# Kernel optimization log

Measured on AMD Instinct MI355X. Metric: run time of the kernel, lower is better.

The kernel has to match this reference:

```python
import jax, jax.numpy as jnp
import numpy as np

N = 100000
E = 1250000
D = 64
EPS = 1e-12


def lgconv(x, edge_index):
    # PyG LGConv: symmetric gcn_norm WITHOUT self-loops, scatter-add to target.
    src, dst = edge_index[0], edge_index[1]
    n = x.shape[0]
    deg = jax.ops.segment_sum(jnp.ones((edge_index.shape[1],), x.dtype), dst, num_segments=n)
    dinv = jnp.where(deg > 0, jax.lax.rsqrt(jnp.maximum(deg, 1.0)) * (deg > 0), 0.0)
    dinv = jnp.where(deg > 0, deg ** -0.5, 0.0)
    norm = dinv[src] * dinv[dst]                      # [E]
    msgs = norm[:, None] * x[src]                     # [E, D]
    return jax.ops.segment_sum(msgs, dst, num_segments=n)


def l2_normalize(x):
    # torch F.normalize(dim=1): x / max(||x||_2, eps)
    nrm = jnp.sqrt(jnp.sum(x * x, axis=1, keepdims=True))
    return x / jnp.maximum(nrm, EPS)


def setup_inputs() -> dict:
    key = jax.random.key(0)
    ks = jax.random.split(key, 8)
    return {
        "init_feat": jax.random.normal(ks[0], (N, D), jnp.float32),
        "W1": jax.random.normal(ks[1], (3 * D, 128), jnp.float32) * (1.0 / np.sqrt(3 * D)),
        "b1": jnp.zeros((128,), jnp.float32),
        "W2": jax.random.normal(ks[2], (128, 3), jnp.float32) * (1.0 / np.sqrt(128)),
        "b2": jnp.zeros((3,), jnp.float32),
        "edge_index_title": jax.random.randint(ks[3], (2, E), 0, N, jnp.int32),
        "edge_index_year": jax.random.randint(ks[4], (2, E), 0, N, jnp.int32),
        "edge_index_cat": jax.random.randint(ks[5], (2, E), 0, N, jnp.int32),
    }


def reference(init_feat, W1, b1, W2, b2, edge_index_title, edge_index_year, edge_index_cat):
    x_title = init_feat
    for _ in range(2):
        x_title = lgconv(x_title, edge_index_title)
    x_title = l2_normalize(x_title)

    x_year = lgconv(init_feat, edge_index_year)
    x_year = l2_normalize(x_year)

    x_cat = init_feat
    for _ in range(3):
        x_cat = lgconv(x_cat, edge_index_cat)
    x_cat = l2_normalize(x_cat)

    x_all = jnp.concatenate([x_title, x_year, x_cat], axis=1)  # [N, 3D]
    h = jax.nn.relu(x_all @ W1 + b1)
    att = jax.nn.softmax(h @ W2 + b2, axis=1)                  # [N, 3]
    out = att[:, 0:1] * x_title + att[:, 1:2] * x_year + att[:, 2:3] * x_cat
    return out
```

## Files before the change

### kernel.cpp

```cpp
#include <hip/hip_runtime.h>


constexpr int NN = 100000;
constexpr int NE = 1250000;
constexpr int BROWS = 128;
constexpr int NB = (NN + BROWS - 1) / BROWS;
constexpr int CHUNK = 8192;
constexpr int NCHUNK = (NE + CHUNK - 1) / CHUNK;

typedef short bf16x8 __attribute__((ext_vector_type(8)));
typedef short bf16x4 __attribute__((ext_vector_type(4)));
typedef float f32x4 __attribute__((ext_vector_type(4)));

__device__ inline short f2bf(float f) {
    unsigned u = __builtin_bit_cast(unsigned, f);
    u += 0x7FFFu + ((u >> 16) & 1u);
    return (short)(u >> 16);
}

__global__ __launch_bounds__(256) void k_bhist(const int* __restrict__ e0, const int* __restrict__ e1,
                                               const int* __restrict__ e2, int* __restrict__ btot) {
    __shared__ int hist[NB];
    const int tid = threadIdx.x;
    const int set = blockIdx.x / NCHUNK;
    const int chunk = blockIdx.x % NCHUNK;
    const int* ei = (set == 0) ? e0 : (set == 1) ? e1 : e2;
    const int ebase = chunk * CHUNK;
    for (int b = tid; b < NB; b += 256) hist[b] = 0;
    __syncthreads();
    #pragma unroll
    for (int j = 0; j < CHUNK / 256; ++j) {
        int e = ebase + tid + j * 256;
        if (e < NE) atomicAdd(&hist[ei[NE + e] >> 7], 1);
    }
    __syncthreads();
    for (int b = tid; b < NB; b += 256) {
        int h = hist[b];
        if (h > 0) atomicAdd(&btot[set * NB + b], h);
    }
}

__global__ __launch_bounds__(256) void k_bscan2(const int* __restrict__ btot,
                                                int* __restrict__ bstart, int* __restrict__ gcur) {
    const int tid = threadIdx.x;
    if (tid >= 64) return;
    for (int s = 0; s < 3; ++s) {
        int run = 0;
        for (int base = 0; base < NB; base += 64) {
            int idx = base + tid;
            int v = (idx < NB) ? btot[s * NB + idx] : 0;
            int incl = v;
            #pragma unroll
            for (int off = 1; off < 64; off <<= 1) {
                int u = __shfl_up(incl, off);
                if (tid >= off) incl += u;
            }
            if (idx < NB) {
                int st = run + incl - v;
                bstart[s * NB + idx] = st;
                gcur[s * NB + idx] = st;
            }
            run += __shfl(incl, 63);
        }
    }
}

__global__ __launch_bounds__(256) void k_bscat(const int* __restrict__ e0, const int* __restrict__ e1,
                                               const int* __restrict__ e2,
                                               int* __restrict__ gcur, int* __restrict__ gpacked) {
    __shared__ int lpack[CHUNK];
    __shared__ unsigned short lbkt[CHUNK];
    __shared__ int hist[NB];
    __shared__ int lbase[NB];
    __shared__ int lcur[NB];
    const int tid = threadIdx.x;
    const int set = blockIdx.x / NCHUNK;
    const int chunk = blockIdx.x % NCHUNK;
    const int* ei = (set == 0) ? e0 : (set == 1) ? e1 : e2;
    const int ebase = chunk * CHUNK;

    for (int b = tid; b < NB; b += 256) { hist[b] = 0; lcur[b] = 0; }
    __syncthreads();

    #pragma unroll
    for (int j = 0; j < CHUNK / 256; ++j) {
        int k = tid + j * 256;
        int e = ebase + k;
        if (e < NE) {
            int s = ei[e];
            int d = ei[NE + e];
            int b = d >> 7;
            lpack[k] = ((d & 127) << 17) | s;
            lbkt[k] = (unsigned short)b;
            atomicAdd(&hist[b], 1);
        } else {
            lbkt[k] = 0xFFFFu;
        }
    }
    __syncthreads();
    for (int b = tid; b < NB; b += 256) {
        int h = hist[b];
        if (h > 0) lbase[b] = atomicAdd(&gcur[set * NB + b], h);
    }
    __syncthreads();
    int* gp = gpacked + (size_t)set * NE;
    #pragma unroll
    for (int j = 0; j < CHUNK / 256; ++j) {
        int k = tid + j * 256;
        unsigned short b = lbkt[k];
        if (b != 0xFFFFu) {
            int pos = lbase[b] + atomicAdd(&lcur[b], 1);
            gp[pos] = lpack[k];
        }
    }
}

__global__ __launch_bounds__(256) void k_bfin(const int* __restrict__ gpacked,
                                              const int* __restrict__ bstart,
                                              const int* __restrict__ gcur,
                                              int* __restrict__ cnt, float* __restrict__ dinv,
                                              int* __restrict__ rowstart, int* __restrict__ csr) {
    __shared__ int hist[BROWS];
    __shared__ int rst[BROWS];
    __shared__ int lcur[BROWS];
    const int tid = threadIdx.x;
    const int set = blockIdx.x / NB, b = blockIdx.x % NB;
    if (tid < BROWS) { hist[tid] = 0; lcur[tid] = 0; }
    __syncthreads();

    const int base = bstart[set * NB + b];
    const int n = gcur[set * NB + b] - base;
    const int* gp = gpacked + (size_t)set * NE + base;

    for (int k = tid; k < n; k += 256) atomicAdd(&hist[(gp[k] >> 17) & 127], 1);
    __syncthreads();

    if (tid < 64) {
        int v0 = hist[tid], v1 = hist[64 + tid];
        int i0 = v0;
        #pragma unroll
        for (int off = 1; off < 64; off <<= 1) {
            int u = __shfl_up(i0, off);
            if (tid >= off) i0 += u;
        }
        int t0 = __shfl(i0, 63);
        int i1 = v1;
        #pragma unroll
        for (int off = 1; off < 64; off <<= 1) {
            int u = __shfl_up(i1, off);
            if (tid >= off) i1 += u;
        }
        rst[tid] = base + i0 - v0;
        rst[64 + tid] = base + t0 + i1 - v1;
    }
    __syncthreads();

    if (tid < BROWS) {
        int node = b * BROWS + tid;
        if (node < NN) {
            int c = hist[tid];
            cnt[set * NN + node] = c;
            dinv[set * NN + node] = (c > 0) ? (1.0f / sqrtf((float)c)) : 0.0f;
            rowstart[set * NN + node] = rst[tid];
        }
    }

    int* cs = csr + (size_t)set * NE;
    for (int k = tid; k < n; k += 256) {
        int p = gp[k];
        int d = (p >> 17) & 127;
        int pos = rst[d] + atomicAdd(&lcur[d], 1);
        cs[pos] = p & 0x1FFFF;
    }
}

__global__ __launch_bounds__(256) void k_prep(const float* __restrict__ W1, short* __restrict__ W1t) {
    int idx = blockIdx.x * 256 + threadIdx.x;
    if (idx < 128 * 192) {
        int n = idx & 127, k = idx >> 7;
        W1t[n * 192 + k] = f2bf(W1[k * 128 + n]);
    }
}

template<bool PRE, bool SQOUT>
__global__ __launch_bounds__(256) void k_gather(const float* __restrict__ x, float* __restrict__ y,
                                                const int* __restrict__ csr, const int* __restrict__ rowstart,
                                                const int* __restrict__ cnt, const float* __restrict__ dinv) {
    const int node = blockIdx.x * 4 + (threadIdx.x >> 6);
    const int lane = threadIdx.x & 63;
    const int sub = lane >> 4;
    const int fq = lane & 15;
    const int n = cnt[node];
    float a0 = 0.f, a1 = 0.f, a2 = 0.f, a3 = 0.f;
    if (n > 0) {
        const int* lst = csr + rowstart[node];
        for (int i = sub; i < n; i += 16) {
            const int j1 = i + 4, j2 = i + 8, j3 = i + 12;
            const int s0 = lst[i];
            const int s1 = lst[j1 < n ? j1 : n - 1];
            const int s2 = lst[j2 < n ? j2 : n - 1];
            const int s3 = lst[j3 < n ? j3 : n - 1];
            float w0, w1, w2, w3;
            if (PRE) {
                w0 = 1.f;
                w1 = (j1 < n) ? 1.f : 0.f;
                w2 = (j2 < n) ? 1.f : 0.f;
                w3 = (j3 < n) ? 1.f : 0.f;
            } else {
                w0 = dinv[s0];
                w1 = (j1 < n) ? dinv[s1] : 0.f;
                w2 = (j2 < n) ? dinv[s2] : 0.f;
                w3 = (j3 < n) ? dinv[s3] : 0.f;
            }
            const float4 v0 = *(const float4*)(x + (size_t)s0 * 64 + fq * 4);
            const float4 v1 = *(const float4*)(x + (size_t)s1 * 64 + fq * 4);
            const float4 v2 = *(const float4*)(x + (size_t)s2 * 64 + fq * 4);
            const float4 v3 = *(const float4*)(x + (size_t)s3 * 64 + fq * 4);
            a0 = fmaf(w0, v0.x, a0); a1 = fmaf(w0, v0.y, a1);
            a2 = fmaf(w0, v0.z, a2); a3 = fmaf(w0, v0.w, a3);
            a0 = fmaf(w1, v1.x, a0); a1 = fmaf(w1, v1.y, a1);
            a2 = fmaf(w1, v1.z, a2); a3 = fmaf(w1, v1.w, a3);
            a0 = fmaf(w2, v2.x, a0); a1 = fmaf(w2, v2.y, a1);
            a2 = fmaf(w2, v2.z, a2); a3 = fmaf(w2, v2.w, a3);
            a0 = fmaf(w3, v3.x, a0); a1 = fmaf(w3, v3.y, a1);
            a2 = fmaf(w3, v3.z, a2); a3 = fmaf(w3, v3.w, a3);
        }
    }
    a0 += __shfl_xor(a0, 16); a1 += __shfl_xor(a1, 16);
    a2 += __shfl_xor(a2, 16); a3 += __shfl_xor(a3, 16);
    a0 += __shfl_xor(a0, 32); a1 += __shfl_xor(a1, 32);
    a2 += __shfl_xor(a2, 32); a3 += __shfl_xor(a3, 32);
    if (sub == 0) {
        float dn = dinv[node];
        float sc = SQOUT ? dn * dn : dn;
        *(float4*)(y + (size_t)node * 64 + fq * 4) =
            make_float4(sc * a0, sc * a1, sc * a2, sc * a3);
    }
}

constexpr int XROW = 200;

__global__ __launch_bounds__(256) void k_final(const float* __restrict__ xt, const float* __restrict__ xy,
                                               const float* __restrict__ xc, const short* __restrict__ W1t,
                                               const float* __restrict__ b1, const float* __restrict__ W2,
                                               const float* __restrict__ b2, float* __restrict__ out) {
    __shared__ alignas(16) short Xn[64 * XROW];
    __shared__ float rnorm[3 * 64];
    __shared__ float attw[64][4];
    const int tid = threadIdx.x;
    const int wid = tid >> 6, lane = tid & 63;
    const int slot = lane >> 4, fq = lane & 15;
    const int m0 = wid * 16;
    const int nbase = blockIdx.x * 64;

    #pragma unroll
    for (int it = 0; it < 12; ++it) {
        int idx = it * 4 + slot;
        int br = idx >> 4, noff = idx & 15;
        int m = m0 + noff;
        int nodeg = nbase + m;
        const float* xp = (br == 0) ? xt : (br == 1) ? xy : xc;
        float4 v = make_float4(0.f, 0.f, 0.f, 0.f);
        if (nodeg < NN) v = *(const float4*)(xp + (size_t)nodeg * 64 + fq * 4);
        float ss = v.x * v.x + v.y * v.y + v.z * v.z + v.w * v.w;
        #pragma unroll
        for (int off = 8; off > 0; off >>= 1) ss += __shfl_xor(ss, off);
        float rn = 1.0f / fmaxf(sqrtf(ss), 1e-12f);
        bf16x4 s4;
        s4[0] = f2bf(v.x * rn); s4[1] = f2bf(v.y * rn);
        s4[2] = f2bf(v.z * rn); s4[3] = f2bf(v.w * rn);
        *(bf16x4*)&Xn[m * XROW + br * 64 + fq * 4] = s4;
        if (fq == 0) rnorm[br * 64 + m] = rn;
    }
    __syncthreads();

    const int mrow = lane & 15, g = lane >> 4;
    bf16x8 afr[6];
    #pragma unroll
    for (int kk = 0; kk < 6; ++kk)
        afr[kk] = *(const bf16x8*)&Xn[(m0 + mrow) * XROW + kk * 32 + g * 8];
    f32x4 acc[8];
    #pragma unroll
    for (int nt = 0; nt < 8; ++nt) acc[nt] = (f32x4){0.f, 0.f, 0.f, 0.f};
    #pragma unroll
    for (int nt = 0; nt < 8; ++nt) {
        const short* wp = W1t + (nt * 16 + mrow) * 192 + g * 8;
        #pragma unroll
        for (int kk = 0; kk < 6; ++kk)
            acc[nt] = __builtin_amdgcn_mfma_f32_16x16x32_bf16(
                afr[kk], *(const bf16x8*)(wp + kk * 32), acc[nt], 0, 0, 0);
    }
    float p[4][3] = {};
    #pragma unroll
    for (int nt = 0; nt < 8; ++nt) {
        int col = nt * 16 + mrow;
        float b1v = b1[col];
        float w20 = W2[col * 3 + 0], w21 = W2[col * 3 + 1], w22 = W2[col * 3 + 2];
        #pragma unroll
        for (int i = 0; i < 4; ++i) {
            float h = fmaxf(acc[nt][i] + b1v, 0.f);
            p[i][0] = fmaf(h, w20, p[i][0]);
            p[i][1] = fmaf(h, w21, p[i][1]);
            p[i][2] = fmaf(h, w22, p[i][2]);
        }
    }
    #pragma unroll
    for (int i = 0; i < 4; ++i)
        #pragma unroll
        for (int off = 8; off > 0; off >>= 1) {
            p[i][0] += __shfl_xor(p[i][0], off);
            p[i][1] += __shfl_xor(p[i][1], off);
            p[i][2] += __shfl_xor(p[i][2], off);
        }
    if (mrow == 0) {
        #pragma unroll
        for (int i = 0; i < 4; ++i) {
            int m = m0 + g * 4 + i;
            float l0 = p[i][0] + b2[0], l1 = p[i][1] + b2[1], l2 = p[i][2] + b2[2];
            float mx = fmaxf(l0, fmaxf(l1, l2));
            float e0 = __expf(l0 - mx), e1 = __expf(l1 - mx), e2 = __expf(l2 - mx);
            float inv = 1.0f / (e0 + e1 + e2);
            attw[m][0] = e0 * inv * rnorm[m];
            attw[m][1] = e1 * inv * rnorm[64 + m];
            attw[m][2] = e2 * inv * rnorm[128 + m];
        }
    }
    __syncthreads();

    #pragma unroll
    for (int it = 0; it < 4; ++it) {
        int m = m0 + it * 4 + slot;
        int nodeg = nbase + m;
        if (nodeg < NN) {
            size_t base = (size_t)nodeg * 64 + fq * 4;
            float4 t = *(const float4*)(xt + base);
            float4 y = *(const float4*)(xy + base);
            float4 c = *(const float4*)(xc + base);
            float wt = attw[m][0], wy = attw[m][1], wc = attw[m][2];
            float4 o;
            o.x = wt * t.x + wy * y.x + wc * c.x;
            o.y = wt * t.y + wy * y.y + wc * c.y;
            o.z = wt * t.z + wy * y.z + wc * c.z;
            o.w = wt * t.w + wy * y.w + wc * c.w;
            *(float4*)(out + base) = o;
        }
    }
}

extern "C" void kernel_launch(void* const* d_in, const int* in_sizes, int n_in,
                              void* d_out, int out_size, void* d_ws, size_t ws_size,
                              hipStream_t stream) {
    const float* init_feat = (const float*)d_in[0];
    const float* W1 = (const float*)d_in[1];
    const float* b1 = (const float*)d_in[2];
    const float* W2 = (const float*)d_in[3];
    const float* b2 = (const float*)d_in[4];
    const int* ei[3] = {(const int*)d_in[5], (const int*)d_in[6], (const int*)d_in[7]};

    float* TMP = (float*)d_out;

    float* B1 = (float*)d_ws;
    float* B2 = B1 + (size_t)NN * 64;
    float* dinvA = B2 + (size_t)NN * 64;
    int* cntA = (int*)(dinvA + 3 * NN);
    int* rowA = cntA + 3 * NN;
    int* gpackedA = rowA + 3 * NN;
    int* csrA = gpackedA + (size_t)3 * NE;
    short* W1t = (short*)(csrA + (size_t)3 * NE);
    int* btotA = (int*)(W1t + 128 * 192);
    int* bstartA = btotA + 3 * NB;
    int* gcurA = bstartA + 3 * NB;

    const int TB = 256;
    const int finalGrid = (NN + 63) / 64;

    hipMemsetAsync(btotA, 0, (size_t)(3 * NB) * sizeof(int), stream);

    k_prep<<<(128 * 192 + TB - 1) / TB, TB, 0, stream>>>(W1, W1t);
    k_bhist<<<3 * NCHUNK, TB, 0, stream>>>(ei[0], ei[1], ei[2], btotA);
    k_bscan2<<<1, TB, 0, stream>>>(btotA, bstartA, gcurA);
    k_bscat<<<3 * NCHUNK, TB, 0, stream>>>(ei[0], ei[1], ei[2], gcurA, gpackedA);
    k_bfin<<<3 * NB, TB, 0, stream>>>(gpackedA, bstartA, gcurA, cntA, dinvA, rowA, csrA);

    #define CONV(PRE, SQ, xp, yp, s) \
        k_gather<PRE, SQ><<<NN / 4, TB, 0, stream>>>((xp), (yp), csrA + (size_t)(s) * NE, \
                                                     rowA + (s) * NN, cntA + (s) * NN, dinvA + (s) * NN)
    CONV(false, true,  init_feat, B1, 2);
    CONV(true,  true,  B1,        B2, 2);
    CONV(true,  false, B2,        TMP, 2);
    CONV(false, true,  init_feat, B1, 0);
    CONV(true,  false, B1,        B2, 0);
    CONV(false, false, init_feat, B1, 1);
    #undef CONV

    k_final<<<finalGrid, TB, 0, stream>>>(B2, B1, TMP, W1t, b1, W2, b2, TMP);
}
```

Before: 453.0 us.

## Store features in bf16, batch graph convolutions, and pad bucket CSR

Intermediate node features are stored as bf16 instead of fp32, which halves the bytes moved by the gather-heavy convolutions and the final attention kernel. The separate bucket histogram and scan kernels are replaced by fixed padded buckets of 2048 slots, and the CSR is built in place using a shared-memory window. The three graphs' convolutions are merged into three multi-set gather launches grouped by layer depth. This cuts launch count and bandwidth but loses precision across the stacked layers, and it assumes no bucket ever receives more than 2048 edges.

```diff
diff --git a/kernel.cpp b/kernel.cpp
--- a/kernel.cpp
+++ b/kernel.cpp
@@ -5,11 +5,13 @@
 constexpr int NE = 1250000;
 constexpr int BROWS = 128;
 constexpr int NB = (NN + BROWS - 1) / BROWS;
+constexpr int PADB = 2048;
+constexpr int PADE = NB * PADB;
 constexpr int CHUNK = 8192;
 constexpr int NCHUNK = (NE + CHUNK - 1) / CHUNK;
+constexpr int XROW = 200;
 
 typedef short bf16x8 __attribute__((ext_vector_type(8)));
-typedef short bf16x4 __attribute__((ext_vector_type(4)));
 typedef float f32x4 __attribute__((ext_vector_type(4)));
 
 __device__ inline short f2bf(float f) {
@@ -17,52 +19,41 @@
     u += 0x7FFFu + ((u >> 16) & 1u);
     return (short)(u >> 16);
 }
-
-__global__ __launch_bounds__(256) void k_bhist(const int* __restrict__ e0, const int* __restrict__ e1,
-                                               const int* __restrict__ e2, int* __restrict__ btot) {
-    __shared__ int hist[NB];
-    const int tid = threadIdx.x;
-    const int set = blockIdx.x / NCHUNK;
-    const int chunk = blockIdx.x % NCHUNK;
-    const int* ei = (set == 0) ? e0 : (set == 1) ? e1 : e2;
-    const int ebase = chunk * CHUNK;
-    for (int b = tid; b < NB; b += 256) hist[b] = 0;
-    __syncthreads();
-    #pragma unroll
-    for (int j = 0; j < CHUNK / 256; ++j) {
-        int e = ebase + tid + j * 256;
-        if (e < NE) atomicAdd(&hist[ei[NE + e] >> 7], 1);
-    }
-    __syncthreads();
-    for (int b = tid; b < NB; b += 256) {
-        int h = hist[b];
-        if (h > 0) atomicAdd(&btot[set * NB + b], h);
-    }
-}
-
-__global__ __launch_bounds__(256) void k_bscan2(const int* __restrict__ btot,
-                                                int* __restrict__ bstart, int* __restrict__ gcur) {
-    const int tid = threadIdx.x;
-    if (tid >= 64) return;
-    for (int s = 0; s < 3; ++s) {
-        int run = 0;
-        for (int base = 0; base < NB; base += 64) {
-            int idx = base + tid;
-            int v = (idx < NB) ? btot[s * NB + idx] : 0;
-            int incl = v;
-            #pragma unroll
-            for (int off = 1; off < 64; off <<= 1) {
-                int u = __shfl_up(incl, off);
-                if (tid >= off) incl += u;
-            }
-            if (idx < NB) {
-                int st = run + incl - v;
-                bstart[s * NB + idx] = st;
-                gcur[s * NB + idx] = st;
-            }
-            run += __shfl(incl, 63);
-        }
-    }
+__device__ inline unsigned packbf(float a, float b) {
+    return (unsigned)(unsigned short)f2bf(a) | ((unsigned)(unsigned short)f2bf(b) << 16);
+}
+__device__ inline float bflo(unsigned q) { return __builtin_bit_cast(float, q << 16); }
+__device__ inline float bfhi(unsigned q) { return __builtin_bit_cast(float, q & 0xFFFF0000u); }
+
+__device__ inline void edge_acc(float* acc, uint4 v, float w) {
+    acc[0] = fmaf(w, bflo(v.x), acc[0]); acc[1] = fmaf(w, bfhi(v.x), acc[1]);
+    acc[2] = fmaf(w, bflo(v.y), acc[2]); acc[3] = fmaf(w, bfhi(v.y), acc[3]);
+    acc[4] = fmaf(w, bflo(v.z), acc[4]); acc[5] = fmaf(w, bfhi(v.z), acc[5]);
+    acc[6] = fmaf(w, bflo(v.w), acc[6]); acc[7] = fmaf(w, bfhi(v.w), acc[7]);
+}
+
+__global__ __launch_bounds__(256) void k_tobf(const float* __restrict__ x, unsigned short* __restrict__ o) {
+    int i = blockIdx.x * 256 + threadIdx.x;
+    if (i < NN * 16) {
+        float4 v = ((const float4*)x)[i];
+        uint2 r;
+        r.x = packbf(v.x, v.y);
+        r.y = packbf(v.z, v.w);
+        ((uint2*)o)[i] = r;
+    }
+}
+
+__global__ __launch_bounds__(256) void k_prep(const float* __restrict__ W1, short* __restrict__ W1t) {
+    int idx = blockIdx.x * 256 + threadIdx.x;
+    if (idx < 128 * 192) {
+        int n = idx & 127, k = idx >> 7;
+        W1t[n * 192 + k] = f2bf(W1[k * 128 + n]);
+    }
+}
+
+__global__ __launch_bounds__(256) void k_ginit(int* __restrict__ gcur) {
+    int i = blockIdx.x * 256 + threadIdx.x;
+    if (i < 3 * NB) gcur[i] = (i % NB) * PADB;
 }
 
 __global__ __launch_bounds__(256) void k_bscat(const int* __restrict__ e0, const int* __restrict__ e1,
@@ -103,7 +94,7 @@
         if (h > 0) lbase[b] = atomicAdd(&gcur[set * NB + b], h);
     }
     __syncthreads();
-    int* gp = gpacked + (size_t)set * NE;
+    int* gp = gpacked + (size_t)set * PADE;
     #pragma unroll
     for (int j = 0; j < CHUNK / 256; ++j) {
         int k = tid + j * 256;
@@ -115,11 +106,10 @@
     }
 }
 
-__global__ __launch_bounds__(256) void k_bfin(const int* __restrict__ gpacked,
-                                              const int* __restrict__ bstart,
-                                              const int* __restrict__ gcur,
+__global__ __launch_bounds__(256) void k_bfin(int* __restrict__ gpacked, const int* __restrict__ gcur,
                                               int* __restrict__ cnt, float* __restrict__ dinv,
-                                              int* __restrict__ rowstart, int* __restrict__ csr) {
+                                              int* __restrict__ rowstart) {
+    __shared__ int win[PADB];
     __shared__ int hist[BROWS];
     __shared__ int rst[BROWS];
     __shared__ int lcur[BROWS];
@@ -128,11 +118,15 @@
     if (tid < BROWS) { hist[tid] = 0; lcur[tid] = 0; }
     __syncthreads();
 
-    const int base = bstart[set * NB + b];
+    const int base = b * PADB;
     const int n = gcur[set * NB + b] - base;
-    const int* gp = gpacked + (size_t)set * NE + base;
-
-    for (int k = tid; k < n; k += 256) atomicAdd(&hist[(gp[k] >> 17) & 127], 1);
+    int* gp = gpacked + (size_t)set * PADE + base;
+
+    for (int k = tid; k < n; k += 256) {
+        int p = gp[k];
+        win[k] = p;
+        atomicAdd(&hist[(p >> 17) & 127], 1);
+    }
     __syncthreads();
 
     if (tid < 64) {
@@ -150,8 +144,8 @@
             int u = __shfl_up(i1, off);
             if (tid >= off) i1 += u;
         }
-        rst[tid] = base + i0 - v0;
-        rst[64 + tid] = base + t0 + i1 - v1;
+        rst[tid] = i0 - v0;
+        rst[64 + tid] = t0 + i1 - v1;
     }
     __syncthreads();
 
@@ -161,116 +155,119 @@
             int c = hist[tid];
             cnt[set * NN + node] = c;
             dinv[set * NN + node] = (c > 0) ? (1.0f / sqrtf((float)c)) : 0.0f;
-            rowstart[set * NN + node] = rst[tid];
-        }
-    }
-
-    int* cs = csr + (size_t)set * NE;
+            rowstart[set * NN + node] = base + rst[tid];
+        }
+    }
+
     for (int k = tid; k < n; k += 256) {
-        int p = gp[k];
+        int p = win[k];
         int d = (p >> 17) & 127;
         int pos = rst[d] + atomicAdd(&lcur[d], 1);
-        cs[pos] = p & 0x1FFFF;
-    }
-}
-
-__global__ __launch_bounds__(256) void k_prep(const float* __restrict__ W1, short* __restrict__ W1t) {
-    int idx = blockIdx.x * 256 + threadIdx.x;
-    if (idx < 128 * 192) {
-        int n = idx & 127, k = idx >> 7;
-        W1t[n * 192 + k] = f2bf(W1[k * 128 + n]);
-    }
-}
-
-template<bool PRE, bool SQOUT>
-__global__ __launch_bounds__(256) void k_gather(const float* __restrict__ x, float* __restrict__ y,
-                                                const int* __restrict__ csr, const int* __restrict__ rowstart,
-                                                const int* __restrict__ cnt, const float* __restrict__ dinv) {
-    const int node = blockIdx.x * 4 + (threadIdx.x >> 6);
+        gp[pos] = p & 0x1FFFF;
+    }
+}
+
+struct GA {
+    const unsigned short* x;
+    unsigned short* y;
+    const int* csr;
+    const int* row;
+    const int* cnt;
+    const float* dinv;
+    int pre, sq;
+};
+
+__global__ __launch_bounds__(256) void k_gather3(GA g0, GA g1, GA g2, int perset) {
+    const int bset = blockIdx.x / perset;
+    const int blk = blockIdx.x - bset * perset;
+    const GA ga = (bset == 0) ? g0 : (bset == 1) ? g1 : g2;
+    const int node = blk * 4 + (threadIdx.x >> 6);
     const int lane = threadIdx.x & 63;
-    const int sub = lane >> 4;
-    const int fq = lane & 15;
-    const int n = cnt[node];
-    float a0 = 0.f, a1 = 0.f, a2 = 0.f, a3 = 0.f;
+    const int slot = lane >> 3, fo = lane & 7;
+    const int n = ga.cnt[node];
+    float acc[8] = {0.f, 0.f, 0.f, 0.f, 0.f, 0.f, 0.f, 0.f};
+
     if (n > 0) {
-        const int* lst = csr + rowstart[node];
-        for (int i = sub; i < n; i += 16) {
-            const int j1 = i + 4, j2 = i + 8, j3 = i + 12;
-            const int s0 = lst[i];
-            const int s1 = lst[j1 < n ? j1 : n - 1];
-            const int s2 = lst[j2 < n ? j2 : n - 1];
-            const int s3 = lst[j3 < n ? j3 : n - 1];
-            float w0, w1, w2, w3;
-            if (PRE) {
-                w0 = 1.f;
-                w1 = (j1 < n) ? 1.f : 0.f;
-                w2 = (j2 < n) ? 1.f : 0.f;
-                w3 = (j3 < n) ? 1.f : 0.f;
-            } else {
-                w0 = dinv[s0];
-                w1 = (j1 < n) ? dinv[s1] : 0.f;
-                w2 = (j2 < n) ? dinv[s2] : 0.f;
-                w3 = (j3 < n) ? dinv[s3] : 0.f;
-            }
-            const float4 v0 = *(const float4*)(x + (size_t)s0 * 64 + fq * 4);
-            const float4 v1 = *(const float4*)(x + (size_t)s1 * 64 + fq * 4);
-            const float4 v2 = *(const float4*)(x + (size_t)s2 * 64 + fq * 4);
-            const float4 v3 = *(const float4*)(x + (size_t)s3 * 64 + fq * 4);
-            a0 = fmaf(w0, v0.x, a0); a1 = fmaf(w0, v0.y, a1);
-            a2 = fmaf(w0, v0.z, a2); a3 = fmaf(w0, v0.w, a3);
-            a0 = fmaf(w1, v1.x, a0); a1 = fmaf(w1, v1.y, a1);
-            a2 = fmaf(w1, v1.z, a2); a3 = fmaf(w1, v1.w, a3);
-            a0 = fmaf(w2, v2.x, a0); a1 = fmaf(w2, v2.y, a1);
-            a2 = fmaf(w2, v2.z, a2); a3 = fmaf(w2, v2.w, a3);
-            a0 = fmaf(w3, v3.x, a0); a1 = fmaf(w3, v3.y, a1);
-            a2 = fmaf(w3, v3.z, a2); a3 = fmaf(w3, v3.w, a3);
-        }
-    }
-    a0 += __shfl_xor(a0, 16); a1 += __shfl_xor(a1, 16);
-    a2 += __shfl_xor(a2, 16); a3 += __shfl_xor(a3, 16);
-    a0 += __shfl_xor(a0, 32); a1 += __shfl_xor(a1, 32);
-    a2 += __shfl_xor(a2, 32); a3 += __shfl_xor(a3, 32);
-    if (sub == 0) {
-        float dn = dinv[node];
-        float sc = SQOUT ? dn * dn : dn;
-        *(float4*)(y + (size_t)node * 64 + fq * 4) =
-            make_float4(sc * a0, sc * a1, sc * a2, sc * a3);
-    }
-}
-
-constexpr int XROW = 200;
-
-__global__ __launch_bounds__(256) void k_final(const float* __restrict__ xt, const float* __restrict__ xy,
-                                               const float* __restrict__ xc, const short* __restrict__ W1t,
-                                               const float* __restrict__ b1, const float* __restrict__ W2,
-                                               const float* __restrict__ b2, float* __restrict__ out) {
+        const int* lst = ga.csr + ga.row[node];
+        const bool pre = (ga.pre != 0);
+        int i = slot;
+        for (; i + 8 < n; i += 16) {
+            int s0 = lst[i], s1 = lst[i + 8];
+            float w0 = pre ? 1.f : ga.dinv[s0];
+            float w1 = pre ? 1.f : ga.dinv[s1];
+            uint4 v0 = *(const uint4*)(ga.x + (size_t)s0 * 64 + fo * 8);
+            uint4 v1 = *(const uint4*)(ga.x + (size_t)s1 * 64 + fo * 8);
+            edge_acc(acc, v0, w0);
+            edge_acc(acc, v1, w1);
+        }
+        if (i < n) {
+            int s = lst[i];
+            float w = pre ? 1.f : ga.dinv[s];
+            uint4 v = *(const uint4*)(ga.x + (size_t)s * 64 + fo * 8);
+            edge_acc(acc, v, w);
+        }
+    }
+
+    #pragma unroll
+    for (int off = 8; off < 64; off <<= 1) {
+        #pragma unroll
+        for (int j = 0; j < 8; ++j) acc[j] += __shfl_xor(acc[j], off);
+    }
+    if (slot == 0) {
+        float dn = ga.dinv[node];
+        float sc = ga.sq ? dn * dn : dn;
+        uint4 r;
+        r.x = packbf(sc * acc[0], sc * acc[1]);
+        r.y = packbf(sc * acc[2], sc * acc[3]);
+        r.z = packbf(sc * acc[4], sc * acc[5]);
+        r.w = packbf(sc * acc[6], sc * acc[7]);
+        *(uint4*)(ga.y + (size_t)node * 64 + fo * 8) = r;
+    }
+}
+
+__global__ __launch_bounds__(256) void k_final(const unsigned short* __restrict__ xt,
+                                               const unsigned short* __restrict__ xy,
+                                               const unsigned short* __restrict__ xc,
+                                               const short* __restrict__ W1t,
+                                               const float* __restrict__ b1,
+                                               const float* __restrict__ W2,
+                                               const float* __restrict__ b2,
+                                               float* __restrict__ out) {
     __shared__ alignas(16) short Xn[64 * XROW];
     __shared__ float rnorm[3 * 64];
     __shared__ float attw[64][4];
     const int tid = threadIdx.x;
     const int wid = tid >> 6, lane = tid & 63;
-    const int slot = lane >> 4, fq = lane & 15;
+    const int slot = lane >> 3, fo = lane & 7;
     const int m0 = wid * 16;
     const int nbase = blockIdx.x * 64;
 
     #pragma unroll
-    for (int it = 0; it < 12; ++it) {
-        int idx = it * 4 + slot;
+    for (int it = 0; it < 6; ++it) {
+        int idx = it * 8 + slot;
         int br = idx >> 4, noff = idx & 15;
         int m = m0 + noff;
         int nodeg = nbase + m;
-        const float* xp = (br == 0) ? xt : (br == 1) ? xy : xc;
-        float4 v = make_float4(0.f, 0.f, 0.f, 0.f);
-        if (nodeg < NN) v = *(const float4*)(xp + (size_t)nodeg * 64 + fq * 4);
-        float ss = v.x * v.x + v.y * v.y + v.z * v.z + v.w * v.w;
-        #pragma unroll
-        for (int off = 8; off > 0; off >>= 1) ss += __shfl_xor(ss, off);
+        const unsigned short* xp = (br == 0) ? xt : (br == 1) ? xy : xc;
+        float f[8] = {0.f, 0.f, 0.f, 0.f, 0.f, 0.f, 0.f, 0.f};
+        if (nodeg < NN) {
+            uint4 v = *(const uint4*)(xp + (size_t)nodeg * 64 + fo * 8);
+            f[0] = bflo(v.x); f[1] = bfhi(v.x); f[2] = bflo(v.y); f[3] = bfhi(v.y);
+            f[4] = bflo(v.z); f[5] = bfhi(v.z); f[6] = bflo(v.w); f[7] = bfhi(v.w);
+        }
+        float ss = 0.f;
+        #pragma unroll
+        for (int j = 0; j < 8; ++j) ss = fmaf(f[j], f[j], ss);
+        #pragma unroll
+        for (int off = 1; off < 8; off <<= 1) ss += __shfl_xor(ss, off);
         float rn = 1.0f / fmaxf(sqrtf(ss), 1e-12f);
-        bf16x4 s4;
-        s4[0] = f2bf(v.x * rn); s4[1] = f2bf(v.y * rn);
-        s4[2] = f2bf(v.z * rn); s4[3] = f2bf(v.w * rn);
-        *(bf16x4*)&Xn[m * XROW + br * 64 + fq * 4] = s4;
-        if (fq == 0) rnorm[br * 64 + m] = rn;
+        uint4 r;
+        r.x = packbf(f[0] * rn, f[1] * rn);
+        r.y = packbf(f[2] * rn, f[3] * rn);
+        r.z = packbf(f[4] * rn, f[5] * rn);
+        r.w = packbf(f[6] * rn, f[7] * rn);
+        *(uint4*)&Xn[m * XROW + br * 64 + fo * 8] = r;
+        if (fo == 0) rnorm[br * 64 + m] = rn;
     }
     __syncthreads();
 
@@ -328,21 +325,26 @@
     __syncthreads();
 
     #pragma unroll
-    for (int it = 0; it < 4; ++it) {
-        int m = m0 + it * 4 + slot;
+    for (int it = 0; it < 2; ++it) {
+        int m = m0 + it * 8 + slot;
         int nodeg = nbase + m;
         if (nodeg < NN) {
-            size_t base = (size_t)nodeg * 64 + fq * 4;
-            float4 t = *(const float4*)(xt + base);
-            float4 y = *(const float4*)(xy + base);
-            float4 c = *(const float4*)(xc + base);
+            size_t base = (size_t)nodeg * 64 + fo * 8;
+            uint4 tv = *(const uint4*)(xt + base);
+            uint4 yv = *(const uint4*)(xy + base);
+            uint4 cv = *(const uint4*)(xc + base);
             float wt = attw[m][0], wy = attw[m][1], wc = attw[m][2];
-            float4 o;
-            o.x = wt * t.x + wy * y.x + wc * c.x;
-            o.y = wt * t.y + wy * y.y + wc * c.y;
-            o.z = wt * t.z + wy * y.z + wc * c.z;
-            o.w = wt * t.w + wy * y.w + wc * c.w;
-            *(float4*)(out + base) = o;
+            float4 lo4, hi4;
+            lo4.x = wt * bflo(tv.x) + wy * bflo(yv.x) + wc * bflo(cv.x);
+            lo4.y = wt * bfhi(tv.x) + wy * bfhi(yv.x) + wc * bfhi(cv.x);
+            lo4.z = wt * bflo(tv.y) + wy * bflo(yv.y) + wc * bflo(cv.y);
+            lo4.w = wt * bfhi(tv.y) + wy * bfhi(yv.y) + wc * bfhi(cv.y);
+            hi4.x = wt * bflo(tv.z) + wy * bflo(yv.z) + wc * bflo(cv.z);
+            hi4.y = wt * bfhi(tv.z) + wy * bfhi(yv.z) + wc * bfhi(cv.z);
+            hi4.z = wt * bflo(tv.w) + wy * bflo(yv.w) + wc * bflo(cv.w);
+            hi4.w = wt * bfhi(tv.w) + wy * bfhi(yv.w) + wc * bfhi(cv.w);
+            *(float4*)(out + base) = lo4;
+            *(float4*)(out + base + 4) = hi4;
         }
     }
 }
@@ -357,41 +359,46 @@
     const float* b2 = (const float*)d_in[4];
     const int* ei[3] = {(const int*)d_in[5], (const int*)d_in[6], (const int*)d_in[7]};
 
-    float* TMP = (float*)d_out;
-
-    float* B1 = (float*)d_ws;
-    float* B2 = B1 + (size_t)NN * 64;
-    float* dinvA = B2 + (size_t)NN * 64;
+    unsigned short* P0 = (unsigned short*)d_ws;
+    unsigned short* P1 = P0 + (size_t)NN * 64;
+    unsigned short* P2 = P1 + (size_t)NN * 64;
+    unsigned short* P3 = P2 + (size_t)NN * 64;
+    unsigned short* P4 = P3 + (size_t)NN * 64;
+    float* dinvA = (float*)(P4 + (size_t)NN * 64);
     int* cntA = (int*)(dinvA + 3 * NN);
     int* rowA = cntA + 3 * NN;
     int* gpackedA = rowA + 3 * NN;
-    int* csrA = gpackedA + (size_t)3 * NE;
-    short* W1t = (short*)(csrA + (size_t)3 * NE);
-    int* btotA = (int*)(W1t + 128 * 192);
-    int* bstartA = btotA + 3 * NB;
-    int* gcurA = bstartA + 3 * NB;
+    short* W1t = (short*)(gpackedA + (size_t)3 * PADE);
+    int* gcurA = (int*)(W1t + 128 * 192);
 
     const int TB = 256;
     const int finalGrid = (NN + 63) / 64;
 
-    hipMemsetAsync(btotA, 0, (size_t)(3 * NB) * sizeof(int), stream);
-
+    k_tobf<<<(NN * 16 + TB - 1) / TB, TB, 0, stream>>>(init_feat, P0);
     k_prep<<<(128 * 192 + TB - 1) / TB, TB, 0, stream>>>(W1, W1t);
-    k_bhist<<<3 * NCHUNK, TB, 0, stream>>>(ei[0], ei[1], ei[2], btotA);
-    k_bscan2<<<1, TB, 0, stream>>>(btotA, bstartA, gcurA);
+    k_ginit<<<(3 * NB + TB - 1) / TB, TB, 0, stream>>>(gcurA);
     k_bscat<<<3 * NCHUNK, TB, 0, stream>>>(ei[0], ei[1], ei[2], gcurA, gpackedA);
-    k_bfin<<<3 * NB, TB, 0, stream>>>(gpackedA, bstartA, gcurA, cntA, dinvA, rowA, csrA);
-
-    #define CONV(PRE, SQ, xp, yp, s) \
-        k_gather<PRE, SQ><<<NN / 4, TB, 0, stream>>>((xp), (yp), csrA + (size_t)(s) * NE, \
-                                                     rowA + (s) * NN, cntA + (s) * NN, dinvA + (s) * NN)
-    CONV(false, true,  init_feat, B1, 2);
-    CONV(true,  true,  B1,        B2, 2);
-    CONV(true,  false, B2,        TMP, 2);
-    CONV(false, true,  init_feat, B1, 0);
-    CONV(true,  false, B1,        B2, 0);
-    CONV(false, false, init_feat, B1, 1);
-    #undef CONV
-
-    k_final<<<finalGrid, TB, 0, stream>>>(B2, B1, TMP, W1t, b1, W2, b2, TMP);
-}
+    k_bfin<<<3 * NB, TB, 0, stream>>>(gpackedA, gcurA, cntA, dinvA, rowA);
+
+    #define MKGA(xp, yp, s, PRE, SQ) \
+        GA{ (xp), (yp), gpackedA + (size_t)(s) * PADE, rowA + (s) * NN, \
+            cntA + (s) * NN, dinvA + (s) * NN, (PRE), (SQ) }
+    {
+        GA a0 = MKGA(P0, P1, 2, 0, 1);
+        GA a1 = MKGA(P0, P2, 0, 0, 1);
+        GA a2 = MKGA(P0, P3, 1, 0, 0);
+        k_gather3<<<3 * (NN / 4), TB, 0, stream>>>(a0, a1, a2, NN / 4);
+    }
+    {
+        GA b0 = MKGA(P1, P0, 2, 1, 1);
+        GA b1g = MKGA(P2, P4, 0, 1, 0);
+        k_gather3<<<2 * (NN / 4), TB, 0, stream>>>(b0, b1g, b1g, NN / 4);
+    }
+    {
+        GA c0 = MKGA(P0, P1, 2, 1, 0);
+        k_gather3<<<NN / 4, TB, 0, stream>>>(c0, c0, c0, NN / 4);
+    }
+    #undef MKGA
+
+    k_final<<<finalGrid, TB, 0, stream>>>(P4, P3, P1, W1t, b1, W2, b2, (float*)d_out);
+}
```

New measurement: 384.7 us. 1.18x faster.
